# Kernel tuning notes

Hardware: AMD Instinct MI355X
Metric: run time of the kernel (lower is better)

## Reference

```python
import jax, jax.numpy as jnp
import numpy as np
from jax import lax

EPS = 1e-9

def _squash(v):
    # v: [..., D]; squash nonlinearity from CapsNet
    n = jnp.sum(jnp.square(v), axis=-1, keepdims=True)
    return (n / (1.0 + n) / jnp.sqrt(n + EPS)) * v

def setup_inputs() -> dict:
    key = jax.random.key(0)
    ks = jax.random.split(key, 12)
    B, S, D, NI = 1024, 200, 64, 4
    N_UID, N_MID = 50000, 100000
    return {
        "uid": jax.random.randint(ks[0], (B,), 0, N_UID, dtype=jnp.int32),
        "age": jax.random.randint(ks[1], (B,), 0, N_UID, dtype=jnp.int32),
        "gender": jax.random.randint(ks[2], (B,), 0, N_UID, dtype=jnp.int32),
        "occup": jax.random.randint(ks[3], (B,), 0, N_UID, dtype=jnp.int32),
        "mid_his": jax.random.randint(ks[4], (B, S), 0, N_MID, dtype=jnp.int32),
        "mask": jax.random.randint(ks[5], (B, S), 0, 2).astype(jnp.float32),
        "user_emb_table": jax.random.normal(ks[6], (N_UID, D), jnp.float32) * 0.1,
        "age_table": jax.random.normal(ks[7], (N_UID, D), jnp.float32) * 0.1,
        "gender_table": jax.random.normal(ks[8], (N_UID, D), jnp.float32) * 0.1,
        "occup_table": jax.random.normal(ks[9], (N_UID, D), jnp.float32) * 0.1,
        "mid_emb_table": jax.random.normal(ks[10], (N_MID, D), jnp.float32) * 0.1,
        "w_capsule": jax.random.normal(ks[11], (S, NI * D, D), jnp.float32),
    }

def reference(uid, age, gender, occup, mid_his, mask,
              user_emb_table, age_table, gender_table, occup_table,
              mid_emb_table, w_capsule):
    NI = 4
    B, S = mid_his.shape
    D = mid_emb_table.shape[1]

    # user profile: mean of 4 stacked user feature embeddings
    user_profile = (user_emb_table[uid] + gender_table[gender]
                    + age_table[age] + occup_table[occup]) * 0.25  # [B,D]

    # masked item history embeddings
    item_his = mid_emb_table[mid_his] * mask[:, :, None]  # [B,S,D]

    # adjacency: sigmoid(sum_d h_i[d]*h_j[d]*u[d]) without [B,S,S,D] blowup
    hu = item_his * user_profile[:, None, :]              # [B,S,D]
    adj = jax.nn.sigmoid(jnp.einsum('bid,bjd->bij', hu, item_his))  # [B,S,S]
    adj = adj * mask[:, None, :] * mask[:, :, None]

    # --- CapsuleNetwork, bilinear_type=2 ---
    # TF: sum(w[1,S,NI*D,D] * u[B,S,1,D], axis=3) == contraction over D
    hat = jnp.einsum('bsd,sed->bse', item_his, w_capsule)  # [B,S,NI*D]
    hat = hat.reshape(B, S, NI, D).transpose(0, 2, 1, 3)   # [B,NI,S,D]
    hat_iter = lax.stop_gradient(hat)

    cw = jnp.zeros((B, NI, S), dtype=item_his.dtype)  # routing logits
    atten_mask = mask[:, None, :]                     # [B,1,S] broadcast over NI
    for i in range(3):
        sw = jax.nn.softmax(cw, axis=1)               # softmax over interests
        sw = jnp.where(atten_mask == 0, 0.0, sw)      # [B,NI,S]
        if i < 2:
            cap = _squash(jnp.einsum('bks,bksd->bkd', sw, hat_iter))  # [B,NI,D]
            delta = jnp.einsum('bksd,bkd->bks', hat_iter, cap)
            cw = cw + delta
        else:
            cap = _squash(jnp.einsum('bks,bksd->bkd', sw, hat))
    interest_capsule = cap  # [B,NI,D]; relu_layer=False -> no projection
    return interest_capsule, adj
```

## Files before the change

### kernel.cpp

```cpp
#include <hip/hip_runtime.h>

#define B_SZ 1024
#define S_SZ 200
#define D_SZ 64
#define NI_SZ 4
#define E_SZ 256

using u16 = unsigned short;
using u32 = unsigned int;
typedef short  sh8    __attribute__((ext_vector_type(8)));
typedef __bf16 bf16x8 __attribute__((ext_vector_type(8)));
typedef float  f32x4  __attribute__((ext_vector_type(4)));

__device__ __forceinline__ u16 f2bf(float x) {
  u32 u = __float_as_uint(x);
  u += 0x7FFFu + ((u >> 16) & 1u);
  return (u16)(u >> 16);
}
__device__ __forceinline__ float bf2f(u16 h) {
  return __uint_as_float(((u32)h) << 16);
}
__device__ __forceinline__ bf16x8 ldsw(const u16* arr, int row, int kshort) {
  const int idx = row * 64 + (kshort ^ ((row & 7) << 3));
  return __builtin_bit_cast(bf16x8, *(const sh8*)(arr + idx));
}
__device__ __forceinline__ void stsw(u16* arr, int row, int c, sh8 v) {
  *(sh8*)(arr + row * 64 + 8 * (c ^ (row & 7))) = v;
}

__global__ __launch_bounds__(64) void profile_kernel(
    const int* __restrict__ uid, const int* __restrict__ age,
    const int* __restrict__ gender, const int* __restrict__ occup,
    const float* __restrict__ U, const float* __restrict__ AT,
    const float* __restrict__ GT, const float* __restrict__ OT,
    float* __restrict__ prof)
{
  const int b = blockIdx.x;
  const int d = threadIdx.x;
  float v = U[(size_t)uid[b]   * D_SZ + d]
          + GT[(size_t)gender[b] * D_SZ + d]
          + AT[(size_t)age[b]    * D_SZ + d]
          + OT[(size_t)occup[b]  * D_SZ + d];
  prof[b * D_SZ + d] = 0.25f * v;
}

__global__ __launch_bounds__(256) void wconv_kernel(
    const float* __restrict__ W, u16* __restrict__ Wb)
{
  const int idx = blockIdx.x * 256 + threadIdx.x;
  if (idx >= S_SZ * E_SZ * D_SZ / 8) return;
  const float4 a = *(const float4*)(W + (size_t)idx * 8);
  const float4 b = *(const float4*)(W + (size_t)idx * 8 + 4);
  sh8 r;
  r[0] = (short)f2bf(a.x); r[1] = (short)f2bf(a.y);
  r[2] = (short)f2bf(a.z); r[3] = (short)f2bf(a.w);
  r[4] = (short)f2bf(b.x); r[5] = (short)f2bf(b.y);
  r[6] = (short)f2bf(b.z); r[7] = (short)f2bf(b.w);
  *(sh8*)(Wb + (size_t)idx * 8) = r;
}

__global__ __launch_bounds__(256) void gather_kernel(
    const int* __restrict__ mid_his, const float* __restrict__ mask,
    const float* __restrict__ memb, u16* __restrict__ item_bs)
{
  const int idx = blockIdx.x * 256 + threadIdx.x;
  if (idx >= B_SZ * S_SZ * 8) return;
  const int bs = idx >> 3, d0 = (idx & 7) * 8;
  const float m = mask[bs];
  const float* src = memb + (size_t)mid_his[bs] * D_SZ + d0;
  const float4 a = *(const float4*)(src);
  const float4 b = *(const float4*)(src + 4);
  sh8 r;
  r[0] = (short)f2bf(a.x * m); r[1] = (short)f2bf(a.y * m);
  r[2] = (short)f2bf(a.z * m); r[3] = (short)f2bf(a.w * m);
  r[4] = (short)f2bf(b.x * m); r[5] = (short)f2bf(b.y * m);
  r[6] = (short)f2bf(b.z * m); r[7] = (short)f2bf(b.w * m);
  *(sh8*)(item_bs + (size_t)bs * D_SZ + d0) = r;
}

__global__ __launch_bounds__(256, 3) void adj_mfma(
    const u16* __restrict__ item_bs, const float* __restrict__ prof,
    const float* __restrict__ mask, float* __restrict__ adj)
{
  const int b = blockIdx.x;
  __shared__ u16 Hs[208 * 64];
  __shared__ u16 Us[208 * 64];
  __shared__ float Ms[208];
  const int tid = threadIdx.x;

  for (int idx = tid; idx < 208 * 8; idx += 256) {
    const int row = idx >> 3, c = idx & 7;
    sh8 v, h;
    if (row < S_SZ) {
      v = *(const sh8*)(item_bs + ((size_t)b * S_SZ + row) * D_SZ + c * 8);
      const float4 p0 = *(const float4*)(prof + b * D_SZ + c * 8);
      const float4 p1 = *(const float4*)(prof + b * D_SZ + c * 8 + 4);
      const float pv[8] = {p0.x, p0.y, p0.z, p0.w, p1.x, p1.y, p1.z, p1.w};
      #pragma unroll
      for (int j = 0; j < 8; j++)
        h[j] = (short)f2bf(bf2f((u16)v[j]) * pv[j]);
    } else {
      #pragma unroll
      for (int j = 0; j < 8; j++) { v[j] = 0; h[j] = 0; }
    }
    stsw(Hs, row, c, v);
    stsw(Us, row, c, h);
  }
  if (tid < 208) Ms[tid] = (tid < S_SZ) ? mask[b * S_SZ + tid] : 0.f;
  __syncthreads();

  const int w = tid >> 6, l = tid & 63;
  const int lr = l & 15, lg = l >> 4;
  float* outb = adj + (size_t)b * S_SZ * S_SZ;

  for (int mt = 0; mt < 13; mt++) {
    const int arow = mt * 16 + lr;
    const bf16x8 a0 = ldsw(Us, arow, lg * 8);
    const bf16x8 a1 = ldsw(Us, arow, 32 + lg * 8);
    for (int nt = w; nt < 13; nt += 4) {
      const int brow = nt * 16 + lr;
      const bf16x8 b0 = ldsw(Hs, brow, lg * 8);
      const bf16x8 b1 = ldsw(Hs, brow, 32 + lg * 8);
      f32x4 acc = {0.f, 0.f, 0.f, 0.f};
      acc = __builtin_amdgcn_mfma_f32_16x16x32_bf16(a0, b0, acc, 0, 0, 0);
      acc = __builtin_amdgcn_mfma_f32_16x16x32_bf16(a1, b1, acc, 0, 0, 0);
      const int n = nt * 16 + lr;
      const float mj = Ms[n];
      #pragma unroll
      for (int r = 0; r < 4; r++) {
        const int m = mt * 16 + lg * 4 + r;
        if (m < S_SZ && n < S_SZ) {
          const float sg = 1.f / (1.f + __expf(-acc[r]));
          outb[(size_t)m * S_SZ + n] = sg * Ms[m] * mj;
        }
      }
    }
  }
}

__global__ __launch_bounds__(256, 4) void hat_mfma(
    const u16* __restrict__ item_bs, const u16* __restrict__ Wb,
    u16* __restrict__ hatb)
{
  const int s  = blockIdx.x;
  const int b0 = blockIdx.y * 64;
  __shared__ u16 As[64 * 64];
  __shared__ u16 Ws_[256 * 64];
  const int tid = threadIdx.x;

  for (int idx = tid; idx < 64 * 8; idx += 256) {
    const int row = idx >> 3, c = idx & 7;
    const sh8 v = *(const sh8*)(item_bs + ((size_t)(b0 + row) * S_SZ + s) * D_SZ + c * 8);
    stsw(As, row, c, v);
  }
  for (int idx = tid; idx < 256 * 8; idx += 256) {
    const int row = idx >> 3, c = idx & 7;
    const sh8 v = *(const sh8*)(Wb + ((size_t)s * E_SZ + row) * D_SZ + c * 8);
    stsw(Ws_, row, c, v);
  }
  __syncthreads();

  const int w = tid >> 6, l = tid & 63;
  const int lr = l & 15, lg = l >> 4;

  f32x4 acc[4][4];
  #pragma unroll
  for (int mt = 0; mt < 4; mt++)
    #pragma unroll
    for (int nt = 0; nt < 4; nt++) acc[mt][nt] = (f32x4){0.f, 0.f, 0.f, 0.f};

  #pragma unroll
  for (int ks = 0; ks < 2; ks++) {
    bf16x8 af[4], bf_[4];
    #pragma unroll
    for (int mt = 0; mt < 4; mt++)
      af[mt] = ldsw(As, mt * 16 + lr, ks * 32 + lg * 8);
    #pragma unroll
    for (int nt = 0; nt < 4; nt++)
      bf_[nt] = ldsw(Ws_, w * 64 + nt * 16 + lr, ks * 32 + lg * 8);
    #pragma unroll
    for (int mt = 0; mt < 4; mt++)
      #pragma unroll
      for (int nt = 0; nt < 4; nt++)
        acc[mt][nt] = __builtin_amdgcn_mfma_f32_16x16x32_bf16(af[mt], bf_[nt], acc[mt][nt], 0, 0, 0);
  }

  #pragma unroll
  for (int mt = 0; mt < 4; mt++) {
    #pragma unroll
    for (int r = 0; r < 4; r++) {
      const int bb = b0 + mt * 16 + lg * 4 + r;
      u16* dst = hatb + (((size_t)bb * NI_SZ + w) * S_SZ + s) * D_SZ;
      #pragma unroll
      for (int nt = 0; nt < 4; nt++)
        dst[nt * 16 + lr] = f2bf(acc[mt][nt][r]);
    }
  }
}

__device__ __forceinline__ float rlane(float v, int l) {
  return __int_as_float(__builtin_amdgcn_readlane(__float_as_int(v), l));
}

__global__ __launch_bounds__(1024, 4) void route_kernel(
    const u16* __restrict__ hatb, const float* __restrict__ mask,
    float* __restrict__ out)
{
  const int b = blockIdx.x;
  const int t = threadIdx.x;
  const int w = t >> 6, lane = t & 63;
  const int k = w >> 2, q = w & 3;
  __shared__ float cwS[NI_SZ][212];
  __shared__ float partS[NI_SZ][4][D_SZ];

  const float msv = (lane < 50) ? mask[b * S_SZ + q * 50 + lane] : 0.f;

  float hr[50];
  const u16* hg = hatb + (((size_t)b * NI_SZ + k) * S_SZ + q * 50) * D_SZ + lane;
  #pragma unroll
  for (int j = 0; j < 50; j++) hr[j] = bf2f(hg[j * D_SZ]);
  #pragma unroll
  for (int j = 0; j < 50; j++) asm volatile("" : "+v"(hr[j]));

  const int jj = __brev(lane) >> 26;

  for (int iter = 0; iter < 3; ++iter) {
    float swv;
    if (iter == 0) {
      swv = 0.25f * msv;
    } else {
      const int sidx = q * 50 + (lane < 50 ? lane : 49);
      const float a0 = cwS[0][sidx], a1 = cwS[1][sidx],
                  a2 = cwS[2][sidx], a3 = cwS[3][sidx];
      const float mx = fmaxf(fmaxf(a0, a1), fmaxf(a2, a3));
      const float e0 = __expf(a0 - mx), e1 = __expf(a1 - mx),
                  e2 = __expf(a2 - mx), e3 = __expf(a3 - mx);
      const float ek = (k == 0) ? e0 : (k == 1) ? e1 : (k == 2) ? e2 : e3;
      const float inv = 1.f / (e0 + e1 + e2 + e3);
      swv = (msv == 0.f) ? 0.f : ek * inv;
    }

    float c0 = 0.f, c1 = 0.f, c2 = 0.f, c3 = 0.f;
    #pragma unroll
    for (int j = 0; j < 48; j += 4) {
      c0 = fmaf(rlane(swv, j + 0), hr[j + 0], c0);
      c1 = fmaf(rlane(swv, j + 1), hr[j + 1], c1);
      c2 = fmaf(rlane(swv, j + 2), hr[j + 2], c2);
      c3 = fmaf(rlane(swv, j + 3), hr[j + 3], c3);
    }
    c0 = fmaf(rlane(swv, 48), hr[48], c0);
    c1 = fmaf(rlane(swv, 49), hr[49], c1);
    partS[k][q][lane] = (c0 + c2) + (c1 + c3);
    __syncthreads();

    const float cap = partS[k][0][lane] + partS[k][1][lane]
                    + partS[k][2][lane] + partS[k][3][lane];
    float n = cap * cap;
    #pragma unroll
    for (int off = 32; off; off >>= 1) n += __shfl_xor(n, off);
    const float f = n / (1.f + n) * rsqrtf(n + 1e-9f);
    const float capd = cap * f;

    if (iter < 2) {
      float p[32];
      {
        const int bit = lane & 1;
        #pragma unroll
        for (int j = 0; j < 32; j++) {
          const float lo = hr[j] * capd;
          const float hi = (j + 32 < 50) ? hr[j + 32] * capd : 0.f;
          const float send = bit ? lo : hi;
          const float keep = bit ? hi : lo;
          p[j] = keep + __shfl_xor(send, 1);
        }
      }
      #pragma unroll
      for (int r = 1; r < 6; r++) {
        const int dist = 1 << r;
        const int half = 32 >> r;
        const int bit = (lane >> r) & 1;
        #pragma unroll
        for (int j = 0; j < 32; j++) {
          if (j < half) {
            const float send = bit ? p[j] : p[j + half];
            const float keep = bit ? p[j + half] : p[j];
            p[j] = keep + __shfl_xor(send, dist);
          }
        }
      }
      if (jj < 50) {
        if (iter == 0) cwS[k][q * 50 + jj] = p[0];
        else           cwS[k][q * 50 + jj] += p[0];
      }
      __syncthreads();
    } else if (q == 0) {
      out[((size_t)b * NI_SZ + k) * D_SZ + lane] = capd;
    }
  }
}

extern "C" void kernel_launch(void* const* d_in, const int* in_sizes, int n_in,
                              void* d_out, int out_size, void* d_ws, size_t ws_size,
                              hipStream_t stream)
{
  const int*   uid     = (const int*)d_in[0];
  const int*   age     = (const int*)d_in[1];
  const int*   gender  = (const int*)d_in[2];
  const int*   occup   = (const int*)d_in[3];
  const int*   mid_his = (const int*)d_in[4];
  const float* mask    = (const float*)d_in[5];
  const float* U       = (const float*)d_in[6];
  const float* AT      = (const float*)d_in[7];
  const float* GT      = (const float*)d_in[8];
  const float* OT      = (const float*)d_in[9];
  const float* ME      = (const float*)d_in[10];
  const float* WC      = (const float*)d_in[11];

  float* out  = (float*)d_out;
  float* adj  = out + B_SZ * NI_SZ * D_SZ;

  char* ws = (char*)d_ws;
  float* prof    = (float*)ws;
  u16*   item_bs = (u16*)(ws + 262144);
  u16*   Wb      = (u16*)(ws + 262144 + 26214400);
  u16*   hatb    = (u16*)(ws + 262144 + 26214400 + 6553600);

  profile_kernel<<<B_SZ, 64, 0, stream>>>(uid, age, gender, occup, U, AT, GT, OT, prof);
  wconv_kernel<<<(S_SZ * E_SZ * D_SZ / 8 + 255) / 256, 256, 0, stream>>>(WC, Wb);
  gather_kernel<<<(B_SZ * S_SZ * 8 + 255) / 256, 256, 0, stream>>>(mid_his, mask, ME, item_bs);
  adj_mfma<<<B_SZ, 256, 0, stream>>>(item_bs, prof, mask, adj);
  hat_mfma<<<dim3(S_SZ, 16), 256, 0, stream>>>(item_bs, Wb, hatb);
  route_kernel<<<B_SZ, 1024, 0, stream>>>(hatb, mask, out);
}
```

Before: 167.7 us.

## Fuse profile and gather kernels into adj kernel, compute hu in registers

Merges the user-profile and item-gather kernels into the adjacency kernel. Each block now gathers its own item embeddings, writes them to the workspace for the hat kernel, and builds the profile vector in shared memory. The profile-scaled operand is formed in registers from the single shared tile, which removes the second LDS buffer and allows higher occupancy. The change also uses nontemporal stores for the large adj output and swaps the hat grid dimensions so consecutive blocks share the same s weights. Risks are a longer serial gather phase inside each adj block and less parallelism in the gather than the old standalone kernel had.

```diff
diff --git a/kernel.cpp b/kernel.cpp
--- a/kernel.cpp
+++ b/kernel.cpp
@@ -20,28 +20,15 @@
 __device__ __forceinline__ float bf2f(u16 h) {
   return __uint_as_float(((u32)h) << 16);
 }
+__device__ __forceinline__ sh8 ldsr(const u16* arr, int row, int kshort) {
+  const int idx = row * 64 + (kshort ^ ((row & 7) << 3));
+  return *(const sh8*)(arr + idx);
+}
 __device__ __forceinline__ bf16x8 ldsw(const u16* arr, int row, int kshort) {
-  const int idx = row * 64 + (kshort ^ ((row & 7) << 3));
-  return __builtin_bit_cast(bf16x8, *(const sh8*)(arr + idx));
+  return __builtin_bit_cast(bf16x8, ldsr(arr, row, kshort));
 }
 __device__ __forceinline__ void stsw(u16* arr, int row, int c, sh8 v) {
   *(sh8*)(arr + row * 64 + 8 * (c ^ (row & 7))) = v;
-}
-
-__global__ __launch_bounds__(64) void profile_kernel(
-    const int* __restrict__ uid, const int* __restrict__ age,
-    const int* __restrict__ gender, const int* __restrict__ occup,
-    const float* __restrict__ U, const float* __restrict__ AT,
-    const float* __restrict__ GT, const float* __restrict__ OT,
-    float* __restrict__ prof)
-{
-  const int b = blockIdx.x;
-  const int d = threadIdx.x;
-  float v = U[(size_t)uid[b]   * D_SZ + d]
-          + GT[(size_t)gender[b] * D_SZ + d]
-          + AT[(size_t)age[b]    * D_SZ + d]
-          + OT[(size_t)occup[b]  * D_SZ + d];
-  prof[b * D_SZ + d] = 0.25f * v;
 }
 
 __global__ __launch_bounds__(256) void wconv_kernel(
@@ -59,64 +46,72 @@
   *(sh8*)(Wb + (size_t)idx * 8) = r;
 }
 
-__global__ __launch_bounds__(256) void gather_kernel(
+__global__ __launch_bounds__(256, 4) void adj_fused(
+    const int* __restrict__ uid, const int* __restrict__ age,
+    const int* __restrict__ gender, const int* __restrict__ occup,
+    const float* __restrict__ U, const float* __restrict__ AT,
+    const float* __restrict__ GT, const float* __restrict__ OT,
     const int* __restrict__ mid_his, const float* __restrict__ mask,
-    const float* __restrict__ memb, u16* __restrict__ item_bs)
-{
-  const int idx = blockIdx.x * 256 + threadIdx.x;
-  if (idx >= B_SZ * S_SZ * 8) return;
-  const int bs = idx >> 3, d0 = (idx & 7) * 8;
-  const float m = mask[bs];
-  const float* src = memb + (size_t)mid_his[bs] * D_SZ + d0;
-  const float4 a = *(const float4*)(src);
-  const float4 b = *(const float4*)(src + 4);
-  sh8 r;
-  r[0] = (short)f2bf(a.x * m); r[1] = (short)f2bf(a.y * m);
-  r[2] = (short)f2bf(a.z * m); r[3] = (short)f2bf(a.w * m);
-  r[4] = (short)f2bf(b.x * m); r[5] = (short)f2bf(b.y * m);
-  r[6] = (short)f2bf(b.z * m); r[7] = (short)f2bf(b.w * m);
-  *(sh8*)(item_bs + (size_t)bs * D_SZ + d0) = r;
-}
-
-__global__ __launch_bounds__(256, 3) void adj_mfma(
-    const u16* __restrict__ item_bs, const float* __restrict__ prof,
-    const float* __restrict__ mask, float* __restrict__ adj)
+    const float* __restrict__ memb,
+    u16* __restrict__ item_bs, float* __restrict__ adj)
 {
   const int b = blockIdx.x;
-  __shared__ u16 Hs[208 * 64];
-  __shared__ u16 Us[208 * 64];
+  __shared__ u16   Hs[208 * 64];
   __shared__ float Ms[208];
+  __shared__ int   midS[S_SZ];
+  __shared__ float pS[D_SZ];
   const int tid = threadIdx.x;
 
-  for (int idx = tid; idx < 208 * 8; idx += 256) {
+  if (tid < 208) Ms[tid] = (tid < S_SZ) ? mask[b * S_SZ + tid] : 0.f;
+  if (tid < S_SZ) midS[tid] = mid_his[b * S_SZ + tid];
+  if (tid < D_SZ) {
+    float v = U[(size_t)uid[b]    * D_SZ + tid]
+            + GT[(size_t)gender[b] * D_SZ + tid]
+            + AT[(size_t)age[b]    * D_SZ + tid]
+            + OT[(size_t)occup[b]  * D_SZ + tid];
+    pS[tid] = 0.25f * v;
+  }
+  __syncthreads();
+
+  for (int idx = tid; idx < S_SZ * 8; idx += 256) {
     const int row = idx >> 3, c = idx & 7;
-    sh8 v, h;
-    if (row < S_SZ) {
-      v = *(const sh8*)(item_bs + ((size_t)b * S_SZ + row) * D_SZ + c * 8);
-      const float4 p0 = *(const float4*)(prof + b * D_SZ + c * 8);
-      const float4 p1 = *(const float4*)(prof + b * D_SZ + c * 8 + 4);
-      const float pv[8] = {p0.x, p0.y, p0.z, p0.w, p1.x, p1.y, p1.z, p1.w};
-      #pragma unroll
-      for (int j = 0; j < 8; j++)
-        h[j] = (short)f2bf(bf2f((u16)v[j]) * pv[j]);
-    } else {
-      #pragma unroll
-      for (int j = 0; j < 8; j++) { v[j] = 0; h[j] = 0; }
-    }
+    const float m = Ms[row];
+    const float* src = memb + (size_t)midS[row] * D_SZ + c * 8;
+    const float4 a = *(const float4*)(src);
+    const float4 d = *(const float4*)(src + 4);
+    sh8 v;
+    v[0] = (short)f2bf(a.x * m); v[1] = (short)f2bf(a.y * m);
+    v[2] = (short)f2bf(a.z * m); v[3] = (short)f2bf(a.w * m);
+    v[4] = (short)f2bf(d.x * m); v[5] = (short)f2bf(d.y * m);
+    v[6] = (short)f2bf(d.z * m); v[7] = (short)f2bf(d.w * m);
     stsw(Hs, row, c, v);
-    stsw(Us, row, c, h);
-  }
-  if (tid < 208) Ms[tid] = (tid < S_SZ) ? mask[b * S_SZ + tid] : 0.f;
+    *(sh8*)(item_bs + ((size_t)b * S_SZ + row) * D_SZ + c * 8) = v;
+  }
+  if (tid < 64) {
+    sh8 z = {0,0,0,0,0,0,0,0};
+    stsw(Hs, S_SZ + (tid >> 3), tid & 7, z);
+  }
   __syncthreads();
 
   const int w = tid >> 6, l = tid & 63;
   const int lr = l & 15, lg = l >> 4;
+  float pvA[8], pvB[8];
+  #pragma unroll
+  for (int j = 0; j < 8; j++) { pvA[j] = pS[lg * 8 + j]; pvB[j] = pS[32 + lg * 8 + j]; }
+
   float* outb = adj + (size_t)b * S_SZ * S_SZ;
-
   for (int mt = 0; mt < 13; mt++) {
     const int arow = mt * 16 + lr;
-    const bf16x8 a0 = ldsw(Us, arow, lg * 8);
-    const bf16x8 a1 = ldsw(Us, arow, 32 + lg * 8);
+    const sh8 r0 = ldsr(Hs, arow, lg * 8);
+    const sh8 r1 = ldsr(Hs, arow, 32 + lg * 8);
+    sh8 h0, h1;
+    #pragma unroll
+    for (int j = 0; j < 8; j++) {
+      h0[j] = (short)f2bf(bf2f((u16)r0[j]) * pvA[j]);
+      h1[j] = (short)f2bf(bf2f((u16)r1[j]) * pvB[j]);
+    }
+    const bf16x8 a0 = __builtin_bit_cast(bf16x8, h0);
+    const bf16x8 a1 = __builtin_bit_cast(bf16x8, h1);
     for (int nt = w; nt < 13; nt += 4) {
       const int brow = nt * 16 + lr;
       const bf16x8 b0 = ldsw(Hs, brow, lg * 8);
@@ -131,7 +126,7 @@
         const int m = mt * 16 + lg * 4 + r;
         if (m < S_SZ && n < S_SZ) {
           const float sg = 1.f / (1.f + __expf(-acc[r]));
-          outb[(size_t)m * S_SZ + n] = sg * Ms[m] * mj;
+          __builtin_nontemporal_store(sg * Ms[m] * mj, &outb[(size_t)m * S_SZ + n]);
         }
       }
     }
@@ -142,8 +137,8 @@
     const u16* __restrict__ item_bs, const u16* __restrict__ Wb,
     u16* __restrict__ hatb)
 {
-  const int s  = blockIdx.x;
-  const int b0 = blockIdx.y * 64;
+  const int s  = blockIdx.y;
+  const int b0 = blockIdx.x * 64;
   __shared__ u16 As[64 * 64];
   __shared__ u16 Ws_[256 * 64];
   const int tid = threadIdx.x;
@@ -320,15 +315,13 @@
   float* adj  = out + B_SZ * NI_SZ * D_SZ;
 
   char* ws = (char*)d_ws;
-  float* prof    = (float*)ws;
-  u16*   item_bs = (u16*)(ws + 262144);
-  u16*   Wb      = (u16*)(ws + 262144 + 26214400);
-  u16*   hatb    = (u16*)(ws + 262144 + 26214400 + 6553600);
-
-  profile_kernel<<<B_SZ, 64, 0, stream>>>(uid, age, gender, occup, U, AT, GT, OT, prof);
+  u16*   item_bs = (u16*)ws;
+  u16*   Wb      = (u16*)(ws + 26214400);
+  u16*   hatb    = (u16*)(ws + 26214400 + 6553600);
+
   wconv_kernel<<<(S_SZ * E_SZ * D_SZ / 8 + 255) / 256, 256, 0, stream>>>(WC, Wb);
-  gather_kernel<<<(B_SZ * S_SZ * 8 + 255) / 256, 256, 0, stream>>>(mid_his, mask, ME, item_bs);
-  adj_mfma<<<B_SZ, 256, 0, stream>>>(item_bs, prof, mask, adj);
-  hat_mfma<<<dim3(S_SZ, 16), 256, 0, stream>>>(item_bs, Wb, hatb);
+  adj_fused<<<B_SZ, 256, 0, stream>>>(uid, age, gender, occup, U, AT, GT, OT,
+                                      mid_his, mask, ME, item_bs, adj);
+  hat_mfma<<<dim3(16, S_SZ), 256, 0, stream>>>(item_bs, Wb, hatb);
   route_kernel<<<B_SZ, 1024, 0, stream>>>(hatb, mask, out);
 }
```

Result: slower. 231.6 us (+38.1%).
